# Kernel tuning notes

Measured on AMD Instinct MI355X. Metric: run time of the kernel, lower is better.

Reference implementation:

```python
import jax, jax.numpy as jnp
import numpy as np

B, T, N, C = 32, 16, 256, 192
S, D = 8, 192          # num_slots, slot_dim (tokens_per_slot=1 * token_dim=192)
ITERS = 3
EPS = 1e-8
SCALE = D ** -0.5


def _ln(x, g, b):
    mu = jnp.mean(x, axis=-1, keepdims=True)
    var = jnp.var(x, axis=-1, keepdims=True)
    return (x - mu) * jax.lax.rsqrt(var + 1e-5) * g + b


def setup_inputs() -> dict:
    key = jax.random.key(0)
    ks = jax.random.split(key, 20)
    def xav(k, shape):
        fan_in, fan_out = shape[-2], shape[-1]
        lim = np.sqrt(6.0 / (fan_in + fan_out))
        return jax.random.uniform(k, shape, jnp.float32, -lim, lim)
    lim_mu = np.sqrt(6.0 / (1 + D))
    return {
        "inputs": jax.random.normal(ks[0], (B, T, N, C), jnp.float32),
        "noise": jax.random.normal(ks[1], (B, S, D), jnp.float32),
        "slots_mu": jax.random.uniform(ks[2], (1, 1, D), jnp.float32, -lim_mu, lim_mu),
        "slots_log_sigma": jax.random.uniform(ks[3], (1, 1, D), jnp.float32, -lim_mu, lim_mu),
        "ln_in_g": jnp.ones((C,)), "ln_in_b": jnp.zeros((C,)),
        "Wk": xav(ks[4], (C, D)), "Wv": xav(ks[5], (C, D)), "Wq": xav(ks[6], (D, D)),
        "ln_slots_g": jnp.ones((D,)), "ln_slots_b": jnp.zeros((D,)),
        "gru_wih": xav(ks[7], (3 * D, D)),
        "gru_whh": jnp.concatenate([np.linalg.qr(np.random.RandomState(0).randn(D, D))[0].astype(np.float32) for _ in range(3)], axis=0),
        "gru_bih": jnp.zeros((3 * D,)), "gru_bhh": jnp.zeros((3 * D,)),
        "ln_ff_g": jnp.ones((D,)), "ln_ff_b": jnp.zeros((D,)),
        "mlp_w1": xav(ks[8], (D, 4 * D)), "mlp_b1": jnp.zeros((4 * D,)),
        "mlp_w2": xav(ks[9], (4 * D, D)), "mlp_b2": jnp.zeros((D,)),
        "pr_w1": xav(ks[10], (D, D)), "pr_b1": jnp.zeros((D,)),
        "pr_w2": xav(ks[11], (D, D)), "pr_b2": jnp.zeros((D,)),
    }


def reference(inputs, noise, slots_mu, slots_log_sigma, ln_in_g, ln_in_b,
              Wk, Wv, Wq, ln_slots_g, ln_slots_b,
              gru_wih, gru_whh, gru_bih, gru_bhh,
              ln_ff_g, ln_ff_b, mlp_w1, mlp_b1, mlp_w2, mlp_b2,
              pr_w1, pr_b1, pr_w2, pr_b2):
    def gru_cell(x, h):
        gx = x @ gru_wih.T + gru_bih      # [b,S,3D]
        gh = h @ gru_whh.T + gru_bhh
        xr, xz, xn = jnp.split(gx, 3, axis=-1)
        hr, hz, hn = jnp.split(gh, 3, axis=-1)
        r = jax.nn.sigmoid(xr + hr)
        z = jax.nn.sigmoid(xz + hz)
        n = jnp.tanh(xn + r * hn)
        return (1.0 - z) * n + z * h

    x = _ln(inputs, ln_in_g, ln_in_b)                 # [b,T,n,C]
    k = (x @ Wk) * SCALE                              # [b,T,n,D]
    v = x @ Wv
    slots0 = slots_mu + jnp.exp(slots_log_sigma) * noise  # [b,S,D]

    def step(slots, kv_t):
        k_t, v_t = kv_t                               # [b,n,D]
        dots = None
        for i in range(ITERS):
            slots_prev = slots
            q = _ln(slots, ln_slots_g, ln_slots_b) @ Wq        # [b,S,D]
            dots = jnp.einsum('bnd,bsd->bns', k_t, q)          # [b,n,S]
            attn = jax.nn.softmax(dots, axis=-1) + EPS         # competitive over slots
            attn = attn / jnp.sum(attn, axis=-2, keepdims=True)
            updates = jnp.einsum('bns,bnd->bsd', attn, v_t)
            slots = gru_cell(updates, slots_prev)
            if i < ITERS - 1:
                h = _ln(slots, ln_ff_g, ln_ff_b)
                slots = slots + jax.nn.relu(h @ mlp_w1 + mlp_b1) @ mlp_w2 + mlp_b2
        out_slots = slots
        out_dots = jax.nn.softmax(dots, axis=-1)
        # prior (MLP), pred_prior_from='slots'
        slots = jax.nn.relu(slots @ pr_w1 + pr_b1) @ pr_w2 + pr_b2
        return slots, (out_slots, out_dots)

    kT = jnp.swapaxes(k, 0, 1)                        # [T,b,n,D]
    vT = jnp.swapaxes(v, 0, 1)
    _, (slots_seq, dots_seq) = jax.lax.scan(step, slots0, (kT, vT))
    slots_list = jnp.swapaxes(slots_seq, 0, 1)        # [b,T,S,D]
    dots_list = jnp.swapaxes(dots_seq, 0, 1)          # [b,T,n,S]
    return slots_list, dots_list
```

## Files before the change

kernel.cpp:

```cpp
#include <hip/hip_runtime.h>

typedef __bf16 bf16x8 __attribute__((ext_vector_type(8)));
typedef __bf16 bf16x4 __attribute__((ext_vector_type(4)));
typedef float  f32x4  __attribute__((ext_vector_type(4)));

#define ATTN_EPS 1e-8f
#define K_SCALE  0.07216878364870322f

__device__ __forceinline__ void st_swz(__bf16* buf, int strideB, int row, int col, float v) {
  *(__bf16*)((char*)buf + row * strideB + ((col * 2) ^ ((row & 7) << 4))) = (__bf16)v;
}

template <int KSTEPS>
__device__ __forceinline__ f32x4 mm16(const __bf16* a_lds, int astrideB,
                                      const __bf16* __restrict__ Bg, int ldb,
                                      int n0, int lane) {
  int arow = lane & 15, kgr = lane >> 4;
  const char* ab = (const char*)a_lds + arow * astrideB;
  int aswz = (arow & 7) << 4;
  const __bf16* bp = Bg + (n0 + arow) * ldb + kgr * 8;
  f32x4 acc = {0.f, 0.f, 0.f, 0.f};
#pragma unroll
  for (int ki = 0; ki < KSTEPS; ++ki) {
    bf16x8 a = *(const bf16x8*)(ab + ((ki * 64 + kgr * 16) ^ aswz));
    bf16x8 b = *(const bf16x8*)(bp + ki * 32);
    acc = __builtin_amdgcn_mfma_f32_16x16x32_bf16(a, b, acc, 0, 0, 0);
  }
  return acc;
}

__global__ __launch_bounds__(256) void prep_kernel(
    const float* __restrict__ Wk, const float* __restrict__ Wv, const float* __restrict__ Wq,
    const float* __restrict__ wih, const float* __restrict__ whh,
    const float* __restrict__ w1, const float* __restrict__ w2,
    const float* __restrict__ p1, const float* __restrict__ p2,
    __bf16* __restrict__ WkvP, __bf16* __restrict__ WqP,
    __bf16* __restrict__ wihB, __bf16* __restrict__ whhB,
    __bf16* __restrict__ w1P, __bf16* __restrict__ w2P,
    __bf16* __restrict__ pr1P, __bf16* __restrict__ pr2P) {
  int i = blockIdx.x * 256 + threadIdx.x;
  if (i < 73728) {
    int col = i / 192, c = i - col * 192;
    float v = (col < 192) ? Wk[c * 192 + col] * K_SCALE : Wv[c * 192 + (col - 192)];
    WkvP[i] = (__bf16)v; return;
  }
  i -= 73728;
  if (i < 36864) { int col = i / 192, c = i - col * 192; WqP[i] = (__bf16)Wq[c * 192 + col]; return; }
  i -= 36864;
  if (i < 110592) { wihB[i] = (__bf16)wih[i]; return; }
  i -= 110592;
  if (i < 110592) { whhB[i] = (__bf16)whh[i]; return; }
  i -= 110592;
  if (i < 147456) { int o = i / 192, c = i - o * 192; w1P[i] = (__bf16)w1[c * 768 + o]; return; }
  i -= 147456;
  if (i < 147456) { int o = i / 768, c = i - o * 768; w2P[i] = (__bf16)w2[c * 192 + o]; return; }
  i -= 147456;
  if (i < 36864) { int o = i / 192, c = i - o * 192; pr1P[i] = (__bf16)p1[c * 192 + o]; return; }
  i -= 36864;
  { int o = i / 192, c = i - o * 192; pr2P[i] = (__bf16)p2[c * 192 + o]; }
}

__global__ __launch_bounds__(256) void p1_kernel(
    const float* __restrict__ x_in, const float* __restrict__ lng, const float* __restrict__ lnb,
    const __bf16* __restrict__ Wkv, __bf16* __restrict__ k_all, __bf16* __restrict__ v_all) {
  __shared__ __attribute__((aligned(16))) char pool[64 * 200 * 4];
  __shared__ __attribute__((aligned(16))) __bf16 xh[64 * 192];
  __shared__ float gsh[192], bsh[192];
  float* xs = (float*)pool;
  __bf16* kst = (__bf16*)pool;
  __bf16* vst = (__bf16*)(pool + 24576);

  const int tid = threadIdx.x;
  const int blk = blockIdx.x;
  const long Rbase = (long)blk * 64;
  if (tid < 192) { gsh[tid] = lng[tid]; bsh[tid] = lnb[tid]; }

  const float* gxp = x_in + Rbase * 192;
  for (int i = tid; i < 64 * 48; i += 256) {
    int row = i / 48, c4 = i - row * 48;
    float4 v = *(const float4*)(gxp + row * 192 + c4 * 4);
    float* d = xs + row * 200 + c4 * 4;
    d[0] = v.x; d[1] = v.y; d[2] = v.z; d[3] = v.w;
  }
  __syncthreads();

  const int r = tid >> 2, coff = (tid & 3) * 48;
  float xr[48];
  const float* src = xs + r * 200 + coff;
#pragma unroll
  for (int j = 0; j < 48; j++) xr[j] = src[j];
  float s = 0.f, sq = 0.f;
#pragma unroll
  for (int j = 0; j < 48; j++) { s += xr[j]; sq += xr[j] * xr[j]; }
  s += __shfl_xor(s, 1, 64);  s += __shfl_xor(s, 2, 64);
  sq += __shfl_xor(sq, 1, 64); sq += __shfl_xor(sq, 2, 64);
  float mu = s * (1.f / 192.f);
  float var = sq * (1.f / 192.f) - mu * mu;
  float rs = rsqrtf(var + 1e-5f);
  {
    char* xrow = (char*)xh + r * 384;
    int swz = (r & 7) << 4;
#pragma unroll
    for (int j = 0; j < 6; j++) {
      bf16x8 o;
#pragma unroll
      for (int e = 0; e < 8; e++) {
        int c = coff + j * 8 + e;
        o[e] = (__bf16)((xr[j * 8 + e] - mu) * rs * gsh[c] + bsh[c]);
      }
      *(bf16x8*)(xrow + (((coff + j * 8) * 2) ^ swz)) = o;
    }
  }
  __syncthreads();

  const int w = tid >> 6, lane = tid & 63;
  const int arow = lane & 15, kgr = lane >> 4;
  const int m0 = w * 16;
  const char* ab = (const char*)xh + (m0 + arow) * 384;
  const int aswz = (arow & 7) << 4;

  for (int nt = 0; nt < 12; nt++) {
    int col = nt * 16 + arow;
    const __bf16* bp = Wkv + col * 192 + kgr * 8;
    f32x4 acc = {0.f, 0.f, 0.f, 0.f};
#pragma unroll
    for (int ki = 0; ki < 6; ki++) {
      bf16x8 a = *(const bf16x8*)(ab + ((ki * 64 + kgr * 16) ^ aswz));
      bf16x8 b = *(const bf16x8*)(bp + ki * 32);
      acc = __builtin_amdgcn_mfma_f32_16x16x32_bf16(a, b, acc, 0, 0, 0);
    }
#pragma unroll
    for (int rr = 0; rr < 4; rr++) kst[(m0 + kgr * 4 + rr) * 192 + col] = (__bf16)acc[rr];
  }
  for (int nt = 0; nt < 12; nt++) {
    int dcol = nt * 16 + arow;
    const __bf16* bp = Wkv + (192 + dcol) * 192 + kgr * 8;
    f32x4 acc = {0.f, 0.f, 0.f, 0.f};
#pragma unroll
    for (int ki = 0; ki < 6; ki++) {
      bf16x8 a = *(const bf16x8*)(ab + ((ki * 64 + kgr * 16) ^ aswz));
      bf16x8 b = *(const bf16x8*)(bp + ki * 32);
      acc = __builtin_amdgcn_mfma_f32_16x16x32_bf16(a, b, acc, 0, 0, 0);
    }
    bf16x4 o4;
#pragma unroll
    for (int rr = 0; rr < 4; rr++) o4[rr] = (__bf16)acc[rr];
    *(bf16x4*)(&vst[dcol * 64 + m0 + kgr * 4]) = o4;
  }
  __syncthreads();

  {
    const uint4* s4 = (const uint4*)kst;
    uint4* d4 = (uint4*)(k_all + Rbase * 192);
    for (int i = tid; i < 1536; i += 256) d4[i] = s4[i];
  }
  {
    int bt = blk >> 2;
    int n0g = (blk & 3) * 64;
    __bf16* vout = v_all + (long)bt * 49152 + n0g;
    for (int i = tid; i < 1536; i += 256) {
      int d = i >> 3, cc = i & 7;
      *(uint4*)((char*)(vout + d * 256) + cc * 16) =
          *(const uint4*)((const char*)vst + d * 128 + cc * 16);
    }
  }
}

__global__ __launch_bounds__(1024) void p2_kernel(
    const __bf16* __restrict__ k_all, const __bf16* __restrict__ v_all,
    const __bf16* __restrict__ WqP, const __bf16* __restrict__ wihB, const __bf16* __restrict__ whhB,
    const __bf16* __restrict__ w1P, const __bf16* __restrict__ w2P,
    const __bf16* __restrict__ pr1P, const __bf16* __restrict__ pr2P,
    const float* __restrict__ noise, const float* __restrict__ mu_p, const float* __restrict__ lsig,
    const float* __restrict__ lnsg, const float* __restrict__ lnsb,
    const float* __restrict__ lnfg, const float* __restrict__ lnfb,
    const float* __restrict__ bih, const float* __restrict__ bhh,
    const float* __restrict__ b1p, const float* __restrict__ b2p,
    const float* __restrict__ prb1, const float* __restrict__ prb2,
    float* __restrict__ out) {
  __shared__ __attribute__((aligned(16))) float slots[8 * 192];
  __shared__ __attribute__((aligned(16))) __bf16 slots_bf[16 * 192];
  __shared__ __attribute__((aligned(16))) __bf16 ln_bf[16 * 192];
  __shared__ __attribute__((aligned(16))) __bf16 q_bf[16 * 192];
  __shared__ __attribute__((aligned(16))) __bf16 upd_bf[16 * 192];
  __shared__ __attribute__((aligned(16))) __bf16 attnT[16 * 256];
  __shared__ __attribute__((aligned(16))) __bf16 a_bf[16 * 768];
  __shared__ float gx[8 * 577];
  __shared__ float gh[8 * 577];
  __shared__ float colsum[8];
  __shared__ float Lsg[192], Lsb[192], Lfg[192], Lfb[192];
  __shared__ float Bih[576], Bhh[576], B1s[768], B2s[192], Pb1s[192], Pb2s[192];

  const int tid = threadIdx.x;
  const int w = tid >> 6, lane = tid & 63;
  const int b = blockIdx.x;
  const int kgr = lane >> 4, arow = lane & 15;

  for (int i = tid; i < 192; i += 1024) {
    Lsg[i] = lnsg[i]; Lsb[i] = lnsb[i]; Lfg[i] = lnfg[i]; Lfb[i] = lnfb[i];
    B2s[i] = b2p[i]; Pb1s[i] = prb1[i]; Pb2s[i] = prb2[i];
  }
  for (int i = tid; i < 576; i += 1024) { Bih[i] = bih[i]; Bhh[i] = bhh[i]; }
  for (int i = tid; i < 768; i += 1024) B1s[i] = b1p[i];
  for (int i = tid; i < 16 * 192; i += 1024) {
    slots_bf[i] = (__bf16)0.f; ln_bf[i] = (__bf16)0.f; q_bf[i] = (__bf16)0.f; upd_bf[i] = (__bf16)0.f;
  }
  for (int i = tid; i < 16 * 256; i += 1024) attnT[i] = (__bf16)0.f;
  for (int i = tid; i < 16 * 768; i += 1024) a_bf[i] = (__bf16)0.f;
  __syncthreads();
  for (int i = tid; i < 1536; i += 1024) {
    int s = i / 192, d = i - s * 192;
    float v = mu_p[d] + expf(lsig[d]) * noise[(b * 8 + s) * 192 + d];
    slots[i] = v;
    st_swz(slots_bf, 384, s, d, v);
  }
  __syncthreads();

  float* out_slots = out;
  float* out_dots = out + 786432;

  for (int t = 0; t < 16; ++t) {
    const __bf16* kb = k_all + (long)(b * 16 + t) * 49152;
    const __bf16* vb = v_all + (long)(b * 16 + t) * 49152;
    for (int it = 0; it < 3; ++it) {
      if (tid < 8) colsum[tid] = 0.f;
      if (w < 8) {
        int s = w;
        float v0 = slots[s * 192 + lane], v1 = slots[s * 192 + 64 + lane], v2 = slots[s * 192 + 128 + lane];
        float sm = v0 + v1 + v2, sq = v0 * v0 + v1 * v1 + v2 * v2;
#pragma unroll
        for (int m = 1; m < 64; m <<= 1) { sm += __shfl_xor(sm, m, 64); sq += __shfl_xor(sq, m, 64); }
        float mu = sm * (1.f / 192.f);
        float var = sq * (1.f / 192.f) - mu * mu;
        float rs = rsqrtf(var + 1e-5f);
        st_swz(ln_bf, 384, s, lane,       (v0 - mu) * rs * Lsg[lane]       + Lsb[lane]);
        st_swz(ln_bf, 384, s, lane + 64,  (v1 - mu) * rs * Lsg[lane + 64]  + Lsb[lane + 64]);
        st_swz(ln_bf, 384, s, lane + 128, (v2 - mu) * rs * Lsg[lane + 128] + Lsb[lane + 128]);
      }
      __syncthreads();
      if (w < 12) {
        f32x4 acc = mm16<6>(ln_bf, 384, WqP, 192, w * 16, lane);
        if (kgr < 2) {
          int col = w * 16 + arow;
#pragma unroll
          for (int rr = 0; rr < 4; rr++) st_swz(q_bf, 384, kgr * 4 + rr, col, acc[rr]);
        }
      }
      __syncthreads();
      {
        f32x4 acc = mm16<6>(q_bf, 384, kb, 192, w * 16, lane);
        float m4 = fmaxf(fmaxf(acc[0], acc[1]), fmaxf(acc[2], acc[3]));
        float m8 = fmaxf(m4, __shfl_xor(m4, 16, 64));
        float p0 = __expf(acc[0] - m8), p1 = __expf(acc[1] - m8);
        float p2 = __expf(acc[2] - m8), p3 = __expf(acc[3] - m8);
        float s4 = p0 + p1 + p2 + p3;
        float den = s4 + __shfl_xor(s4, 16, 64);
        float rden = 1.f / den;
        if (kgr < 2) {
          int n = w * 16 + arow;
          float a0 = p0 * rden, a1 = p1 * rden, a2 = p2 * rden, a3 = p3 * rden;
          if (it == 2) {
            float4 o4 = make_float4(a0, a1, a2, a3);
            *(float4*)(out_dots + ((long)(b * 16 + t) * 256 + n) * 8 + kgr * 4) = o4;
          }
          __bf16 e0 = (__bf16)(a0 + ATTN_EPS), e1 = (__bf16)(a1 + ATTN_EPS);
          __bf16 e2 = (__bf16)(a2 + ATTN_EPS), e3 = (__bf16)(a3 + ATTN_EPS);
          int srow = kgr * 4;
          char* base = (char*)attnT;
          *(__bf16*)(base + (srow + 0) * 512 + ((n * 2) ^ (((srow + 0) & 7) << 4))) = e0;
          *(__bf16*)(base + (srow + 1) * 512 + ((n * 2) ^ (((srow + 1) & 7) << 4))) = e1;
          *(__bf16*)(base + (srow + 2) * 512 + ((n * 2) ^ (((srow + 2) & 7) << 4))) = e2;
          *(__bf16*)(base + (srow + 3) * 512 + ((n * 2) ^ (((srow + 3) & 7) << 4))) = e3;
          float c0 = (float)e0, c1 = (float)e1, c2 = (float)e2, c3 = (float)e3;
#pragma unroll
          for (int m = 1; m < 16; m <<= 1) {
            c0 += __shfl_xor(c0, m, 64); c1 += __shfl_xor(c1, m, 64);
            c2 += __shfl_xor(c2, m, 64); c3 += __shfl_xor(c3, m, 64);
          }
          if (arow == 0) {
            atomicAdd(&colsum[srow + 0], c0); atomicAdd(&colsum[srow + 1], c1);
            atomicAdd(&colsum[srow + 2], c2); atomicAdd(&colsum[srow + 3], c3);
          }
        }
      }
      __syncthreads();
      if (w < 12) {
        f32x4 acc = mm16<8>(attnT, 512, vb, 256, w * 16, lane);
        if (kgr < 2) {
          int col = w * 16 + arow;
#pragma unroll
          for (int rr = 0; rr < 4; rr++) {
            int s = kgr * 4 + rr;
            st_swz(upd_bf, 384, s, col, acc[rr] / colsum[s]);
          }
        }
      }
      __syncthreads();
      for (int job = w; job < 72; job += 16) {
        bool isx = job < 36;
        int nt = isx ? job : job - 36;
        f32x4 acc = mm16<6>(isx ? upd_bf : slots_bf, 384, isx ? wihB : whhB, 192, nt * 16, lane);
        if (kgr < 2) {
          int col = nt * 16 + arow;
          float* dst = isx ? gx : gh;
#pragma unroll
          for (int rr = 0; rr < 4; rr++) dst[(kgr * 4 + rr) * 577 + col] = acc[rr];
        }
      }
      __syncthreads();
      for (int i = tid; i < 1536; i += 1024) {
        int s = i / 192, d = i - s * 192;
        float xr_ = gx[s * 577 + d]       + Bih[d];
        float xz_ = gx[s * 577 + 192 + d] + Bih[192 + d];
        float xn_ = gx[s * 577 + 384 + d] + Bih[384 + d];
        float hr_ = gh[s * 577 + d]       + Bhh[d];
        float hz_ = gh[s * 577 + 192 + d] + Bhh[192 + d];
        float hn_ = gh[s * 577 + 384 + d] + Bhh[384 + d];
        float rg = 1.f / (1.f + __expf(-(xr_ + hr_)));
        float zg = 1.f / (1.f + __expf(-(xz_ + hz_)));
        float ng = tanhf(xn_ + rg * hn_);
        float hv = slots[i];
        float nh = (1.f - zg) * ng + zg * hv;
        slots[i] = nh;
        st_swz(slots_bf, 384, s, d, nh);
      }
      __syncthreads();
      if (it < 2) {
        if (w < 8) {
          int s = w;
          float v0 = slots[s * 192 + lane], v1 = slots[s * 192 + 64 + lane], v2 = slots[s * 192 + 128 + lane];
          float sm = v0 + v1 + v2, sq = v0 * v0 + v1 * v1 + v2 * v2;
#pragma unroll
          for (int m = 1; m < 64; m <<= 1) { sm += __shfl_xor(sm, m, 64); sq += __shfl_xor(sq, m, 64); }
          float mu = sm * (1.f / 192.f);
          float var = sq * (1.f / 192.f) - mu * mu;
          float rs = rsqrtf(var + 1e-5f);
          st_swz(ln_bf, 384, s, lane,       (v0 - mu) * rs * Lfg[lane]       + Lfb[lane]);
          st_swz(ln_bf, 384, s, lane + 64,  (v1 - mu) * rs * Lfg[lane + 64]  + Lfb[lane + 64]);
          st_swz(ln_bf, 384, s, lane + 128, (v2 - mu) * rs * Lfg[lane + 128] + Lfb[lane + 128]);
        }
        __syncthreads();
        for (int job = w; job < 48; job += 16) {
          f32x4 acc = mm16<6>(ln_bf, 384, w1P, 192, job * 16, lane);
          if (kgr < 2) {
            int col = job * 16 + arow;
#pragma unroll
            for (int rr = 0; rr < 4; rr++)
              st_swz(a_bf, 1536, kgr * 4 + rr, col, fmaxf(acc[rr] + B1s[col], 0.f));
          }
        }
        __syncthreads();
        if (w < 12) {
          f32x4 acc = mm16<24>(a_bf, 1536, w2P, 768, w * 16, lane);
          if (kgr < 2) {
            int col = w * 16 + arow;
#pragma unroll
            for (int rr = 0; rr < 4; rr++) {
              int s = kgr * 4 + rr;
              float nv = slots[s * 192 + col] + acc[rr] + B2s[col];
              slots[s * 192 + col] = nv;
              st_swz(slots_bf, 384, s, col, nv);
            }
          }
        }
        __syncthreads();
      }
    }
    for (int i = tid; i < 384; i += 1024)
      *(float4*)(out_slots + (long)(b * 16 + t) * 1536 + i * 4) = *(const float4*)(&slots[i * 4]);
    if (w < 12) {
      f32x4 acc = mm16<6>(slots_bf, 384, pr1P, 192, w * 16, lane);
      if (kgr < 2) {
        int col = w * 16 + arow;
#pragma unroll
        for (int rr = 0; rr < 4; rr++)
          st_swz(ln_bf, 384, kgr * 4 + rr, col, fmaxf(acc[rr] + Pb1s[col], 0.f));
      }
    }
    __syncthreads();
    if (w < 12) {
      f32x4 acc = mm16<6>(ln_bf, 384, pr2P, 192, w * 16, lane);
      if (kgr < 2) {
        int col = w * 16 + arow;
#pragma unroll
        for (int rr = 0; rr < 4; rr++) {
          int s = kgr * 4 + rr;
          float nv = acc[rr] + Pb2s[col];
          slots[s * 192 + col] = nv;
          st_swz(slots_bf, 384, s, col, nv);
        }
      }
    }
    __syncthreads();
  }
}

extern "C" void kernel_launch(void* const* d_in, const int* in_sizes, int n_in,
                              void* d_out, int out_size, void* d_ws, size_t ws_size,
                              hipStream_t stream) {
  const float* inputs = (const float*)d_in[0];
  const float* noise  = (const float*)d_in[1];
  const float* mu     = (const float*)d_in[2];
  const float* lsig   = (const float*)d_in[3];
  const float* ln_in_g = (const float*)d_in[4];
  const float* ln_in_b = (const float*)d_in[5];
  const float* Wk = (const float*)d_in[6];
  const float* Wv = (const float*)d_in[7];
  const float* Wq = (const float*)d_in[8];
  const float* lnsg = (const float*)d_in[9];
  const float* lnsb = (const float*)d_in[10];
  const float* wih = (const float*)d_in[11];
  const float* whh = (const float*)d_in[12];
  const float* bih = (const float*)d_in[13];
  const float* bhh = (const float*)d_in[14];
  const float* lnfg = (const float*)d_in[15];
  const float* lnfb = (const float*)d_in[16];
  const float* w1 = (const float*)d_in[17];
  const float* b1 = (const float*)d_in[18];
  const float* w2 = (const float*)d_in[19];
  const float* b2 = (const float*)d_in[20];
  const float* pw1 = (const float*)d_in[21];
  const float* pb1 = (const float*)d_in[22];
  const float* pw2 = (const float*)d_in[23];
  const float* pb2 = (const float*)d_in[24];

  char* ws = (char*)d_ws;
  __bf16* WkvP = (__bf16*)(ws + 0);
  __bf16* WqP  = (__bf16*)(ws + 147456);
  __bf16* wihB = (__bf16*)(ws + 221184);
  __bf16* whhB = (__bf16*)(ws + 442368);
  __bf16* w1P  = (__bf16*)(ws + 663552);
  __bf16* w2P  = (__bf16*)(ws + 958464);
  __bf16* pr1P = (__bf16*)(ws + 1253376);
  __bf16* pr2P = (__bf16*)(ws + 1327104);
  __bf16* k_all = (__bf16*)(ws + 1400832);
  __bf16* v_all = (__bf16*)(ws + 51732480);

  prep_kernel<<<2736, 256, 0, stream>>>(Wk, Wv, Wq, wih, whh, w1, w2, pw1, pw2,
                                        WkvP, WqP, wihB, whhB, w1P, w2P, pr1P, pr2P);
  p1_kernel<<<2048, 256, 0, stream>>>(inputs, ln_in_g, ln_in_b, WkvP, k_all, v_all);
  p2_kernel<<<32, 1024, 0, stream>>>(k_all, v_all, WqP, wihB, whhB, w1P, w2P, pr1P, pr2P,
                                     noise, mu, lsig, lnsg, lnsb, lnfg, lnfb,
                                     bih, bhh, b1, b2, pb1, pb2, (float*)d_out);
}
```

Before: 2.013 ms.

## Overlap GRU hidden matmul with LN and q, compute colsum via MFMA

Restructures the serial per-timestep loop in the recurrent kernel. The GRU hidden-state matmul (gh) is now spread over waves that would otherwise sit idle during the slot LayerNorm and q projection. The attention column sums are computed with an MFMA against a ones matrix instead of shuffles and LDS atomics, and the normalisation is moved into the gx epilogue. The FF LayerNorm is fused into the gate computation, and faster sigmoid/tanh approximations are used. This removes barriers and idle waves on the latency-bound path, at the cost of slightly different numerics (normalising after the matmul, clamped fast tanh).

Measured after the change: 2.117 ms. 1.05x slower.

```diff
diff --git a/kernel.cpp b/kernel.cpp
--- a/kernel.cpp
+++ b/kernel.cpp
@@ -1,32 +1,212 @@
 #include <hip/hip_runtime.h>
 
 typedef __bf16 bf16x8 __attribute__((ext_vector_type(8)));
-typedef __bf16 bf16x4 __attribute__((ext_vector_type(4)));
 typedef float  f32x4  __attribute__((ext_vector_type(4)));
 
 #define ATTN_EPS 1e-8f
 #define K_SCALE  0.07216878364870322f
 
+struct __align__(16) Smem {
+  float slots[8 * 192];
+  __bf16 slots_bf[16 * 192];
+  __bf16 ln_bf[16 * 192];
+  __bf16 q_bf[16 * 192];
+  __bf16 upd_bf[16 * 192];
+  __bf16 attnT[16 * 256];
+  __bf16 a_bf[16 * 768];
+  float gx[8 * 577];
+  float gh[8 * 577];
+  float colsum[8];
+  float Lsg[192], Lsb[192], Lfg[192], Lfb[192];
+  float Bih[576], Bhh[576], B1s[768], B2s[192], Pb1s[192], Pb2s[192];
+};
+
 __device__ __forceinline__ void st_swz(__bf16* buf, int strideB, int row, int col, float v) {
   *(__bf16*)((char*)buf + row * strideB + ((col * 2) ^ ((row & 7) << 4))) = (__bf16)v;
 }
 
-template <int KSTEPS>
-__device__ __forceinline__ f32x4 mm16(const __bf16* a_lds, int astrideB,
-                                      const __bf16* __restrict__ Bg, int ldb,
-                                      int n0, int lane) {
+__device__ __forceinline__ f32x4 zero4() { f32x4 z = {0.f, 0.f, 0.f, 0.f}; return z; }
+
+__device__ __forceinline__ float sigm(float x) {
+  return __builtin_amdgcn_rcpf(1.f + __expf(-x));
+}
+__device__ __forceinline__ float tanhfast(float x) {
+  float a = fminf(12.f, fmaxf(-12.f, x));
+  float e = __expf(2.f * a);
+  return (e - 1.f) * __builtin_amdgcn_rcpf(e + 1.f);
+}
+
+template <int K>
+__device__ __forceinline__ f32x4 mmcore(f32x4 acc, const __bf16* a_lds, int astrideB,
+                                        const __bf16* __restrict__ Bg, int ldb,
+                                        int col0, int kofs, int lane) {
   int arow = lane & 15, kgr = lane >> 4;
   const char* ab = (const char*)a_lds + arow * astrideB;
   int aswz = (arow & 7) << 4;
-  const __bf16* bp = Bg + (n0 + arow) * ldb + kgr * 8;
-  f32x4 acc = {0.f, 0.f, 0.f, 0.f};
-#pragma unroll
-  for (int ki = 0; ki < KSTEPS; ++ki) {
-    bf16x8 a = *(const bf16x8*)(ab + ((ki * 64 + kgr * 16) ^ aswz));
+  const __bf16* bp = Bg + (col0 + arow) * ldb + kofs + kgr * 8;
+#pragma unroll
+  for (int ki = 0; ki < K; ++ki) {
+    bf16x8 a = *(const bf16x8*)(ab + ((kofs * 2 + ki * 64 + kgr * 16) ^ aswz));
     bf16x8 b = *(const bf16x8*)(bp + ki * 32);
     acc = __builtin_amdgcn_mfma_f32_16x16x32_bf16(a, b, acc, 0, 0, 0);
   }
   return acc;
+}
+
+__device__ __forceinline__ void ln_row(Smem& sm, int s, int lane,
+                                       const float* g, const float* bta, __bf16* dst) {
+  float v0 = sm.slots[s * 192 + lane], v1 = sm.slots[s * 192 + 64 + lane], v2 = sm.slots[s * 192 + 128 + lane];
+  float sum = v0 + v1 + v2, sq = v0 * v0 + v1 * v1 + v2 * v2;
+#pragma unroll
+  for (int m = 1; m < 64; m <<= 1) { sum += __shfl_xor(sum, m, 64); sq += __shfl_xor(sq, m, 64); }
+  float mu = sum * (1.f / 192.f);
+  float var = sq * (1.f / 192.f) - mu * mu;
+  float rs = rsqrtf(var + 1e-5f);
+  st_swz(dst, 384, s, lane,       (v0 - mu) * rs * g[lane]       + bta[lane]);
+  st_swz(dst, 384, s, lane + 64,  (v1 - mu) * rs * g[lane + 64]  + bta[lane + 64]);
+  st_swz(dst, 384, s, lane + 128, (v2 - mu) * rs * g[lane + 128] + bta[lane + 128]);
+}
+
+__device__ __forceinline__ void job_gh(Smem& sm, const __bf16* __restrict__ W, int j, int lane) {
+  f32x4 acc = mmcore<6>(zero4(), sm.slots_bf, 384, W, 192, j * 16, 0, lane);
+  int kgr = lane >> 4, arow = lane & 15;
+  if (kgr < 2) {
+    int col = j * 16 + arow;
+#pragma unroll
+    for (int rr = 0; rr < 4; rr++) sm.gh[(kgr * 4 + rr) * 577 + col] = acc[rr];
+  }
+}
+
+__device__ __forceinline__ void job_gx(Smem& sm, const __bf16* __restrict__ W, int j, int lane) {
+  f32x4 acc = mmcore<6>(zero4(), sm.upd_bf, 384, W, 192, j * 16, 0, lane);
+  int kgr = lane >> 4, arow = lane & 15;
+  if (kgr < 2) {
+    int col = j * 16 + arow;
+#pragma unroll
+    for (int rr = 0; rr < 4; rr++) {
+      float sc = __builtin_amdgcn_rcpf(sm.colsum[kgr * 4 + rr]);
+      sm.gx[(kgr * 4 + rr) * 577 + col] = acc[rr] * sc;
+    }
+  }
+}
+
+__device__ __forceinline__ void job_q(Smem& sm, const __bf16* __restrict__ W, int j, int lane) {
+  f32x4 acc = mmcore<6>(zero4(), sm.ln_bf, 384, W, 192, j * 16, 0, lane);
+  int kgr = lane >> 4, arow = lane & 15;
+  if (kgr < 2) {
+    int col = j * 16 + arow;
+#pragma unroll
+    for (int rr = 0; rr < 4; rr++) st_swz(sm.q_bf, 384, kgr * 4 + rr, col, acc[rr]);
+  }
+}
+
+__device__ __forceinline__ void job_upd(Smem& sm, const __bf16* __restrict__ vb, int j, int lane) {
+  f32x4 acc = mmcore<8>(zero4(), sm.attnT, 512, vb, 256, j * 16, 0, lane);
+  int kgr = lane >> 4, arow = lane & 15;
+  if (kgr < 2) {
+    int col = j * 16 + arow;
+#pragma unroll
+    for (int rr = 0; rr < 4; rr++) st_swz(sm.upd_bf, 384, kgr * 4 + rr, col, acc[rr]);
+  }
+}
+
+__device__ __forceinline__ void job_colsum(Smem& sm, const __bf16* __restrict__ onesM, int lane) {
+  f32x4 acc = mmcore<8>(zero4(), sm.attnT, 512, onesM, 256, 0, 0, lane);
+  int kgr = lane >> 4, arow = lane & 15;
+  if (kgr < 2 && arow == 0) {
+#pragma unroll
+    for (int rr = 0; rr < 4; rr++) sm.colsum[kgr * 4 + rr] = acc[rr];
+  }
+}
+
+__device__ __forceinline__ void job_mlp1(Smem& sm, const __bf16* __restrict__ W, int j, int lane) {
+  f32x4 acc = mmcore<6>(zero4(), sm.ln_bf, 384, W, 192, j * 16, 0, lane);
+  int kgr = lane >> 4, arow = lane & 15;
+  if (kgr < 2) {
+    int col = j * 16 + arow;
+#pragma unroll
+    for (int rr = 0; rr < 4; rr++)
+      st_swz(sm.a_bf, 1536, kgr * 4 + rr, col, fmaxf(acc[rr] + sm.B1s[col], 0.f));
+  }
+}
+
+__device__ __forceinline__ void job_mlp2(Smem& sm, const __bf16* __restrict__ W, int j, int lane) {
+  f32x4 acc = zero4();
+#pragma unroll
+  for (int c = 0; c < 4; c++)
+    acc = mmcore<6>(acc, sm.a_bf, 1536, W, 768, j * 16, c * 192, lane);
+  int kgr = lane >> 4, arow = lane & 15;
+  if (kgr < 2) {
+    int col = j * 16 + arow;
+#pragma unroll
+    for (int rr = 0; rr < 4; rr++) {
+      int s = kgr * 4 + rr;
+      float nv = sm.slots[s * 192 + col] + acc[rr] + sm.B2s[col];
+      sm.slots[s * 192 + col] = nv;
+      st_swz(sm.slots_bf, 384, s, col, nv);
+    }
+  }
+}
+
+__device__ __forceinline__ void job_pr1(Smem& sm, const __bf16* __restrict__ W, int j, int lane) {
+  f32x4 acc = mmcore<6>(zero4(), sm.slots_bf, 384, W, 192, j * 16, 0, lane);
+  int kgr = lane >> 4, arow = lane & 15;
+  if (kgr < 2) {
+    int col = j * 16 + arow;
+#pragma unroll
+    for (int rr = 0; rr < 4; rr++)
+      st_swz(sm.ln_bf, 384, kgr * 4 + rr, col, fmaxf(acc[rr] + sm.Pb1s[col], 0.f));
+  }
+}
+
+__device__ __forceinline__ void job_pr2(Smem& sm, const __bf16* __restrict__ W, int j, int lane) {
+  f32x4 acc = mmcore<6>(zero4(), sm.ln_bf, 384, W, 192, j * 16, 0, lane);
+  int kgr = lane >> 4, arow = lane & 15;
+  if (kgr < 2) {
+    int col = j * 16 + arow;
+#pragma unroll
+    for (int rr = 0; rr < 4; rr++) {
+      int s = kgr * 4 + rr;
+      float nv = acc[rr] + sm.Pb2s[col];
+      sm.slots[s * 192 + col] = nv;
+      st_swz(sm.slots_bf, 384, s, col, nv);
+    }
+  }
+}
+
+__device__ __forceinline__ void gates(Smem& sm, int s, int lane, bool lnff) {
+  float nh[3];
+#pragma unroll
+  for (int j = 0; j < 3; j++) {
+    int d = lane + j * 64;
+    float xr = sm.gx[s * 577 + d]       + sm.Bih[d];
+    float xz = sm.gx[s * 577 + 192 + d] + sm.Bih[192 + d];
+    float xn = sm.gx[s * 577 + 384 + d] + sm.Bih[384 + d];
+    float hr = sm.gh[s * 577 + d]       + sm.Bhh[d];
+    float hz = sm.gh[s * 577 + 192 + d] + sm.Bhh[192 + d];
+    float hn = sm.gh[s * 577 + 384 + d] + sm.Bhh[384 + d];
+    float rg = sigm(xr + hr);
+    float zg = sigm(xz + hz);
+    float ng = tanhfast(xn + rg * hn);
+    float hv = sm.slots[s * 192 + d];
+    float v = (1.f - zg) * ng + zg * hv;
+    nh[j] = v;
+    sm.slots[s * 192 + d] = v;
+    st_swz(sm.slots_bf, 384, s, d, v);
+  }
+  if (lnff) {
+    float sum = nh[0] + nh[1] + nh[2], sq = nh[0] * nh[0] + nh[1] * nh[1] + nh[2] * nh[2];
+#pragma unroll
+    for (int m = 1; m < 64; m <<= 1) { sum += __shfl_xor(sum, m, 64); sq += __shfl_xor(sq, m, 64); }
+    float mu = sum * (1.f / 192.f);
+    float var = sq * (1.f / 192.f) - mu * mu;
+    float rs = rsqrtf(var + 1e-5f);
+#pragma unroll
+    for (int j = 0; j < 3; j++) {
+      int d = lane + j * 64;
+      st_swz(sm.ln_bf, 384, s, d, (nh[j] - mu) * rs * sm.Lfg[d] + sm.Lfb[d]);
+    }
+  }
 }
 
 __global__ __launch_bounds__(256) void prep_kernel(
@@ -37,7 +217,8 @@
     __bf16* __restrict__ WkvP, __bf16* __restrict__ WqP,
     __bf16* __restrict__ wihB, __bf16* __restrict__ whhB,
     __bf16* __restrict__ w1P, __bf16* __restrict__ w2P,
-    __bf16* __restrict__ pr1P, __bf16* __restrict__ pr2P) {
+    __bf16* __restrict__ pr1P, __bf16* __restrict__ pr2P,
+    __bf16* __restrict__ onesM) {
   int i = blockIdx.x * 256 + threadIdx.x;
   if (i < 73728) {
     int col = i / 192, c = i - col * 192;
@@ -57,7 +238,9 @@
   i -= 147456;
   if (i < 36864) { int o = i / 192, c = i - o * 192; pr1P[i] = (__bf16)p1[c * 192 + o]; return; }
   i -= 36864;
-  { int o = i / 192, c = i - o * 192; pr2P[i] = (__bf16)p2[c * 192 + o]; }
+  if (i < 36864) { int o = i / 192, c = i - o * 192; pr2P[i] = (__bf16)p2[c * 192 + o]; return; }
+  i -= 36864;
+  if (i < 4096) onesM[i] = (__bf16)1.f;
 }
 
 __global__ __launch_bounds__(256) void p1_kernel(
@@ -142,10 +325,9 @@
       bf16x8 b = *(const bf16x8*)(bp + ki * 32);
       acc = __builtin_amdgcn_mfma_f32_16x16x32_bf16(a, b, acc, 0, 0, 0);
     }
-    bf16x4 o4;
-#pragma unroll
-    for (int rr = 0; rr < 4; rr++) o4[rr] = (__bf16)acc[rr];
-    *(bf16x4*)(&vst[dcol * 64 + m0 + kgr * 4]) = o4;
+    __bf16 o0 = (__bf16)acc[0], o1 = (__bf16)acc[1], o2 = (__bf16)acc[2], o3 = (__bf16)acc[3];
+    __bf16* vp = &vst[dcol * 64 + m0 + kgr * 4];
+    vp[0] = o0; vp[1] = o1; vp[2] = o2; vp[3] = o3;
   }
   __syncthreads();
 
@@ -171,6 +353,7 @@
     const __bf16* __restrict__ WqP, const __bf16* __restrict__ wihB, const __bf16* __restrict__ whhB,
     const __bf16* __restrict__ w1P, const __bf16* __restrict__ w2P,
     const __bf16* __restrict__ pr1P, const __bf16* __restrict__ pr2P,
+    const __bf16* __restrict__ onesM,
     const float* __restrict__ noise, const float* __restrict__ mu_p, const float* __restrict__ lsig,
     const float* __restrict__ lnsg, const float* __restrict__ lnsb,
     const float* __restrict__ lnfg, const float* __restrict__ lnfb,
@@ -178,41 +361,30 @@
     const float* __restrict__ b1p, const float* __restrict__ b2p,
     const float* __restrict__ prb1, const float* __restrict__ prb2,
     float* __restrict__ out) {
-  __shared__ __attribute__((aligned(16))) float slots[8 * 192];
-  __shared__ __attribute__((aligned(16))) __bf16 slots_bf[16 * 192];
-  __shared__ __attribute__((aligned(16))) __bf16 ln_bf[16 * 192];
-  __shared__ __attribute__((aligned(16))) __bf16 q_bf[16 * 192];
-  __shared__ __attribute__((aligned(16))) __bf16 upd_bf[16 * 192];
-  __shared__ __attribute__((aligned(16))) __bf16 attnT[16 * 256];
-  __shared__ __attribute__((aligned(16))) __bf16 a_bf[16 * 768];
-  __shared__ float gx[8 * 577];
-  __shared__ float gh[8 * 577];
-  __shared__ float colsum[8];
-  __shared__ float Lsg[192], Lsb[192], Lfg[192], Lfb[192];
-  __shared__ float Bih[576], Bhh[576], B1s[768], B2s[192], Pb1s[192], Pb2s[192];
-
+  __shared__ Smem sm;
   const int tid = threadIdx.x;
   const int w = tid >> 6, lane = tid & 63;
   const int b = blockIdx.x;
   const int kgr = lane >> 4, arow = lane & 15;
 
   for (int i = tid; i < 192; i += 1024) {
-    Lsg[i] = lnsg[i]; Lsb[i] = lnsb[i]; Lfg[i] = lnfg[i]; Lfb[i] = lnfb[i];
-    B2s[i] = b2p[i]; Pb1s[i] = prb1[i]; Pb2s[i] = prb2[i];
-  }
-  for (int i = tid; i < 576; i += 1024) { Bih[i] = bih[i]; Bhh[i] = bhh[i]; }
-  for (int i = tid; i < 768; i += 1024) B1s[i] = b1p[i];
+    sm.Lsg[i] = lnsg[i]; sm.Lsb[i] = lnsb[i]; sm.Lfg[i] = lnfg[i]; sm.Lfb[i] = lnfb[i];
+    sm.B2s[i] = b2p[i]; sm.Pb1s[i] = prb1[i]; sm.Pb2s[i] = prb2[i];
+  }
+  for (int i = tid; i < 576; i += 1024) { sm.Bih[i] = bih[i]; sm.Bhh[i] = bhh[i]; }
+  for (int i = tid; i < 768; i += 1024) sm.B1s[i] = b1p[i];
   for (int i = tid; i < 16 * 192; i += 1024) {
-    slots_bf[i] = (__bf16)0.f; ln_bf[i] = (__bf16)0.f; q_bf[i] = (__bf16)0.f; upd_bf[i] = (__bf16)0.f;
-  }
-  for (int i = tid; i < 16 * 256; i += 1024) attnT[i] = (__bf16)0.f;
-  for (int i = tid; i < 16 * 768; i += 1024) a_bf[i] = (__bf16)0.f;
+    sm.slots_bf[i] = (__bf16)0.f; sm.ln_bf[i] = (__bf16)0.f;
+    sm.q_bf[i] = (__bf16)0.f; sm.upd_bf[i] = (__bf16)0.f;
+  }
+  for (int i = tid; i < 16 * 256; i += 1024) sm.attnT[i] = (__bf16)0.f;
+  for (int i = tid; i < 16 * 768; i += 1024) sm.a_bf[i] = (__bf16)0.f;
   __syncthreads();
   for (int i = tid; i < 1536; i += 1024) {
     int s = i / 192, d = i - s * 192;
-    float v = mu_p[d] + expf(lsig[d]) * noise[(b * 8 + s) * 192 + d];
-    slots[i] = v;
-    st_swz(slots_bf, 384, s, d, v);
+    float v = mu_p[d] + __expf(lsig[d]) * noise[(b * 8 + s) * 192 + d];
+    sm.slots[i] = v;
+    st_swz(sm.slots_bf, 384, s, d, v);
   }
   __syncthreads();
 
@@ -223,174 +395,59 @@
     const __bf16* kb = k_all + (long)(b * 16 + t) * 49152;
     const __bf16* vb = v_all + (long)(b * 16 + t) * 49152;
     for (int it = 0; it < 3; ++it) {
-      if (tid < 8) colsum[tid] = 0.f;
-      if (w < 8) {
-        int s = w;
-        float v0 = slots[s * 192 + lane], v1 = slots[s * 192 + 64 + lane], v2 = slots[s * 192 + 128 + lane];
-        float sm = v0 + v1 + v2, sq = v0 * v0 + v1 * v1 + v2 * v2;
-#pragma unroll
-        for (int m = 1; m < 64; m <<= 1) { sm += __shfl_xor(sm, m, 64); sq += __shfl_xor(sq, m, 64); }
-        float mu = sm * (1.f / 192.f);
-        float var = sq * (1.f / 192.f) - mu * mu;
-        float rs = rsqrtf(var + 1e-5f);
-        st_swz(ln_bf, 384, s, lane,       (v0 - mu) * rs * Lsg[lane]       + Lsb[lane]);
-        st_swz(ln_bf, 384, s, lane + 64,  (v1 - mu) * rs * Lsg[lane + 64]  + Lsb[lane + 64]);
-        st_swz(ln_bf, 384, s, lane + 128, (v2 - mu) * rs * Lsg[lane + 128] + Lsb[lane + 128]);
-      }
+      if (w < 8) ln_row(sm, w, lane, sm.Lsg, sm.Lsb, sm.ln_bf);
+      else { job_gh(sm, whhB, (w - 8), lane); job_gh(sm, whhB, (w - 8) + 8, lane); }
       __syncthreads();
-      if (w < 12) {
-        f32x4 acc = mm16<6>(ln_bf, 384, WqP, 192, w * 16, lane);
-        if (kgr < 2) {
-          int col = w * 16 + arow;
-#pragma unroll
-          for (int rr = 0; rr < 4; rr++) st_swz(q_bf, 384, kgr * 4 + rr, col, acc[rr]);
-        }
-      }
+      if (w < 12) { job_q(sm, WqP, w, lane); job_gh(sm, whhB, 16 + w, lane); }
+      else { job_gh(sm, whhB, 28 + (w - 12), lane); job_gh(sm, whhB, 32 + (w - 12), lane); }
       __syncthreads();
       {
-        f32x4 acc = mm16<6>(q_bf, 384, kb, 192, w * 16, lane);
+        f32x4 acc = mmcore<6>(zero4(), sm.q_bf, 384, kb, 192, w * 16, 0, lane);
         float m4 = fmaxf(fmaxf(acc[0], acc[1]), fmaxf(acc[2], acc[3]));
         float m8 = fmaxf(m4, __shfl_xor(m4, 16, 64));
         float p0 = __expf(acc[0] - m8), p1 = __expf(acc[1] - m8);
-        float p2 = __expf(acc[2] - m8), p3 = __expf(acc[3] - m8);
-        float s4 = p0 + p1 + p2 + p3;
+        float p2v = __expf(acc[2] - m8), p3 = __expf(acc[3] - m8);
+        float s4 = p0 + p1 + p2v + p3;
         float den = s4 + __shfl_xor(s4, 16, 64);
         float rden = 1.f / den;
         if (kgr < 2) {
           int n = w * 16 + arow;
-          float a0 = p0 * rden, a1 = p1 * rden, a2 = p2 * rden, a3 = p3 * rden;
-          if (it == 2) {
-            float4 o4 = make_float4(a0, a1, a2, a3);
-            *(float4*)(out_dots + ((long)(b * 16 + t) * 256 + n) * 8 + kgr * 4) = o4;
-          }
-          __bf16 e0 = (__bf16)(a0 + ATTN_EPS), e1 = (__bf16)(a1 + ATTN_EPS);
-          __bf16 e2 = (__bf16)(a2 + ATTN_EPS), e3 = (__bf16)(a3 + ATTN_EPS);
-          int srow = kgr * 4;
-          char* base = (char*)attnT;
-          *(__bf16*)(base + (srow + 0) * 512 + ((n * 2) ^ (((srow + 0) & 7) << 4))) = e0;
-          *(__bf16*)(base + (srow + 1) * 512 + ((n * 2) ^ (((srow + 1) & 7) << 4))) = e1;
-          *(__bf16*)(base + (srow + 2) * 512 + ((n * 2) ^ (((srow + 2) & 7) << 4))) = e2;
-          *(__bf16*)(base + (srow + 3) * 512 + ((n * 2) ^ (((srow + 3) & 7) << 4))) = e3;
-          float c0 = (float)e0, c1 = (float)e1, c2 = (float)e2, c3 = (float)e3;
-#pragma unroll
-          for (int m = 1; m < 16; m <<= 1) {
-            c0 += __shfl_xor(c0, m, 64); c1 += __shfl_xor(c1, m, 64);
-            c2 += __shfl_xor(c2, m, 64); c3 += __shfl_xor(c3, m, 64);
-          }
-          if (arow == 0) {
-            atomicAdd(&colsum[srow + 0], c0); atomicAdd(&colsum[srow + 1], c1);
-            atomicAdd(&colsum[srow + 2], c2); atomicAdd(&colsum[srow + 3], c3);
-          }
+          float a0 = p0 * rden, a1 = p1 * rden, a2 = p2v * rden, a3 = p3 * rden;
+          if (it == 2)
+            *(float4*)(out_dots + ((long)(b * 16 + t) * 256 + n) * 8 + kgr * 4) = make_float4(a0, a1, a2, a3);
+          int r0 = kgr * 4;
+          st_swz(sm.attnT, 512, r0 + 0, n, a0 + ATTN_EPS);
+          st_swz(sm.attnT, 512, r0 + 1, n, a1 + ATTN_EPS);
+          st_swz(sm.attnT, 512, r0 + 2, n, a2 + ATTN_EPS);
+          st_swz(sm.attnT, 512, r0 + 3, n, a3 + ATTN_EPS);
         }
       }
       __syncthreads();
-      if (w < 12) {
-        f32x4 acc = mm16<8>(attnT, 512, vb, 256, w * 16, lane);
-        if (kgr < 2) {
-          int col = w * 16 + arow;
-#pragma unroll
-          for (int rr = 0; rr < 4; rr++) {
-            int s = kgr * 4 + rr;
-            st_swz(upd_bf, 384, s, col, acc[rr] / colsum[s]);
-          }
-        }
-      }
+      if (w < 12) job_upd(sm, vb, w, lane);
+      else if (w == 12) job_colsum(sm, onesM, lane);
       __syncthreads();
-      for (int job = w; job < 72; job += 16) {
-        bool isx = job < 36;
-        int nt = isx ? job : job - 36;
-        f32x4 acc = mm16<6>(isx ? upd_bf : slots_bf, 384, isx ? wihB : whhB, 192, nt * 16, lane);
-        if (kgr < 2) {
-          int col = nt * 16 + arow;
-          float* dst = isx ? gx : gh;
-#pragma unroll
-          for (int rr = 0; rr < 4; rr++) dst[(kgr * 4 + rr) * 577 + col] = acc[rr];
-        }
-      }
+      job_gx(sm, wihB, w, lane);
+      job_gx(sm, wihB, w + 16, lane);
+      if (w < 4) job_gx(sm, wihB, w + 32, lane);
       __syncthreads();
-      for (int i = tid; i < 1536; i += 1024) {
-        int s = i / 192, d = i - s * 192;
-        float xr_ = gx[s * 577 + d]       + Bih[d];
-        float xz_ = gx[s * 577 + 192 + d] + Bih[192 + d];
-        float xn_ = gx[s * 577 + 384 + d] + Bih[384 + d];
-        float hr_ = gh[s * 577 + d]       + Bhh[d];
-        float hz_ = gh[s * 577 + 192 + d] + Bhh[192 + d];
-        float hn_ = gh[s * 577 + 384 + d] + Bhh[384 + d];
-        float rg = 1.f / (1.f + __expf(-(xr_ + hr_)));
-        float zg = 1.f / (1.f + __expf(-(xz_ + hz_)));
-        float ng = tanhf(xn_ + rg * hn_);
-        float hv = slots[i];
-        float nh = (1.f - zg) * ng + zg * hv;
-        slots[i] = nh;
-        st_swz(slots_bf, 384, s, d, nh);
-      }
+      if (w < 8) gates(sm, w, lane, it < 2);
       __syncthreads();
       if (it < 2) {
-        if (w < 8) {
-          int s = w;
-          float v0 = slots[s * 192 + lane], v1 = slots[s * 192 + 64 + lane], v2 = slots[s * 192 + 128 + lane];
-          float sm = v0 + v1 + v2, sq = v0 * v0 + v1 * v1 + v2 * v2;
-#pragma unroll
-          for (int m = 1; m < 64; m <<= 1) { sm += __shfl_xor(sm, m, 64); sq += __shfl_xor(sq, m, 64); }
-          float mu = sm * (1.f / 192.f);
-          float var = sq * (1.f / 192.f) - mu * mu;
-          float rs = rsqrtf(var + 1e-5f);
-          st_swz(ln_bf, 384, s, lane,       (v0 - mu) * rs * Lfg[lane]       + Lfb[lane]);
-          st_swz(ln_bf, 384, s, lane + 64,  (v1 - mu) * rs * Lfg[lane + 64]  + Lfb[lane + 64]);
-          st_swz(ln_bf, 384, s, lane + 128, (v2 - mu) * rs * Lfg[lane + 128] + Lfb[lane + 128]);
-        }
+        job_mlp1(sm, w1P, w, lane);
+        job_mlp1(sm, w1P, w + 16, lane);
+        job_mlp1(sm, w1P, w + 32, lane);
         __syncthreads();
-        for (int job = w; job < 48; job += 16) {
-          f32x4 acc = mm16<6>(ln_bf, 384, w1P, 192, job * 16, lane);
-          if (kgr < 2) {
-            int col = job * 16 + arow;
-#pragma unroll
-            for (int rr = 0; rr < 4; rr++)
-              st_swz(a_bf, 1536, kgr * 4 + rr, col, fmaxf(acc[rr] + B1s[col], 0.f));
-          }
-        }
-        __syncthreads();
-        if (w < 12) {
-          f32x4 acc = mm16<24>(a_bf, 1536, w2P, 768, w * 16, lane);
-          if (kgr < 2) {
-            int col = w * 16 + arow;
-#pragma unroll
-            for (int rr = 0; rr < 4; rr++) {
-              int s = kgr * 4 + rr;
-              float nv = slots[s * 192 + col] + acc[rr] + B2s[col];
-              slots[s * 192 + col] = nv;
-              st_swz(slots_bf, 384, s, col, nv);
-            }
-          }
-        }
+        if (w < 12) job_mlp2(sm, w2P, w, lane);
         __syncthreads();
       }
     }
-    for (int i = tid; i < 384; i += 1024)
-      *(float4*)(out_slots + (long)(b * 16 + t) * 1536 + i * 4) = *(const float4*)(&slots[i * 4]);
-    if (w < 12) {
-      f32x4 acc = mm16<6>(slots_bf, 384, pr1P, 192, w * 16, lane);
-      if (kgr < 2) {
-        int col = w * 16 + arow;
-#pragma unroll
-        for (int rr = 0; rr < 4; rr++)
-          st_swz(ln_bf, 384, kgr * 4 + rr, col, fmaxf(acc[rr] + Pb1s[col], 0.f));
-      }
+    if (w < 12) job_pr1(sm, pr1P, w, lane);
+    else {
+      for (int i = (w - 12) * 64 + lane; i < 384; i += 256)
+        *(float4*)(out_slots + (long)(b * 16 + t) * 1536 + i * 4) = *(const float4*)(&sm.slots[i * 4]);
     }
     __syncthreads();
-    if (w < 12) {
-      f32x4 acc = mm16<6>(ln_bf, 384, pr2P, 192, w * 16, lane);
-      if (kgr < 2) {
-        int col = w * 16 + arow;
-#pragma unroll
-        for (int rr = 0; rr < 4; rr++) {
-          int s = kgr * 4 + rr;
-          float nv = acc[rr] + Pb2s[col];
-          slots[s * 192 + col] = nv;
-          st_swz(slots_bf, 384, s, col, nv);
-        }
-      }
-    }
+    if (w < 12) job_pr2(sm, pr2P, w, lane);
     __syncthreads();
   }
 }
@@ -435,11 +492,12 @@
   __bf16* pr2P = (__bf16*)(ws + 1327104);
   __bf16* k_all = (__bf16*)(ws + 1400832);
   __bf16* v_all = (__bf16*)(ws + 51732480);
-
-  prep_kernel<<<2736, 256, 0, stream>>>(Wk, Wv, Wq, wih, whh, w1, w2, pw1, pw2,
-                                        WkvP, WqP, wihB, whhB, w1P, w2P, pr1P, pr2P);
+  __bf16* onesM = (__bf16*)(ws + 102064128);
+
+  prep_kernel<<<2752, 256, 0, stream>>>(Wk, Wv, Wq, wih, whh, w1, w2, pw1, pw2,
+                                        WkvP, WqP, wihB, whhB, w1P, w2P, pr1P, pr2P, onesM);
   p1_kernel<<<2048, 256, 0, stream>>>(inputs, ln_in_g, ln_in_b, WkvP, k_all, v_all);
-  p2_kernel<<<32, 1024, 0, stream>>>(k_all, v_all, WqP, wihB, whhB, w1P, w2P, pr1P, pr2P,
+  p2_kernel<<<32, 1024, 0, stream>>>(k_all, v_all, WqP, wihB, whhB, w1P, w2P, pr1P, pr2P, onesM,
                                      noise, mu, lsig, lnsg, lnsb, lnfg, lnfb,
                                      bih, bhh, b1, b2, pb1, pb2, (float*)d_out);
 }
```
